# Kernel optimization log

Measured on AMD Instinct MI355X. Metric: run time of the kernel, lower is better.

Reference implementation:

```python
import jax, jax.numpy as jnp
import numpy as np
import math

D = 512
H = 8
DH = D // H
B, T = 4, 2048


def _poly(x, coeffs):
    # iterative-power polynomial eval, same products as the Vandermonde matmul
    acc = coeffs[0] * jnp.ones_like(x)
    p = jnp.ones_like(x)
    for i in range(1, coeffs.shape[0]):
        p = p * x
        acc = acc + coeffs[i] * p
    return acc


def _exp_fn(x, exp_c):
    return jnp.maximum(_poly(x, exp_c), 1e-8)


def _softmax(x, exp_c):
    x = x - jnp.max(x, axis=-1, keepdims=True)
    e = _exp_fn(x, exp_c)
    return e / jnp.sum(e, axis=-1, keepdims=True)


def _gelu(x, gelu_c):
    return _poly(jnp.clip(x, -4.0, 4.0), gelu_c)


def _layernorm(x, gamma, beta):
    mean = jnp.mean(x, axis=-1, keepdims=True)
    var = jnp.mean(x * x, axis=-1, keepdims=True) - mean * mean
    v = var + 1e-5
    y = jnp.full_like(v, 0.5)
    for _ in range(3):  # Newton iterations for rsqrt
        y = y * (3.0 - v * y * y) * 0.5
    return (x - mean) * y * gamma + beta


def setup_inputs() -> dict:
    key = jax.random.key(0)
    ks = jax.random.split(key, 8)
    x = jax.random.normal(ks[0], (B, T, D), dtype=jnp.float32)
    s = 0.02
    Wq = jax.random.normal(ks[1], (D, D), dtype=jnp.float32) * s
    Wk = jax.random.normal(ks[2], (D, D), dtype=jnp.float32) * s
    Wv = jax.random.normal(ks[3], (D, D), dtype=jnp.float32) * s
    Wo = jax.random.normal(ks[4], (D, D), dtype=jnp.float32) * s
    W1 = jax.random.normal(ks[5], (D, 4 * D), dtype=jnp.float32) * s
    W2 = jax.random.normal(ks[6], (4 * D, D), dtype=jnp.float32) * s
    g1 = jnp.ones((D,), jnp.float32); b1 = jnp.zeros((D,), jnp.float32)
    g2 = jnp.ones((D,), jnp.float32); b2 = jnp.zeros((D,), jnp.float32)
    # GELU degree-7 least-squares fit on [-4,4]
    x_fit = jnp.linspace(-4.0, 4.0, 1000)
    y_fit = 0.5 * x_fit * (1.0 + jax.scipy.special.erf(x_fit / math.sqrt(2.0)))
    V = x_fit[:, None] ** jnp.arange(8)[None, :]
    gelu_c = jnp.linalg.lstsq(V, y_fit)[0].astype(jnp.float32)
    # exp Taylor coeffs degree 6
    exp_c = jnp.array([1.0 / math.factorial(i) for i in range(7)], dtype=jnp.float32)
    return dict(x=x, Wq=Wq, Wk=Wk, Wv=Wv, Wo=Wo, W1=W1, W2=W2,
                g1=g1, b1=b1, g2=g2, b2=b2, gelu_c=gelu_c, exp_c=exp_c)


def reference(x, Wq, Wk, Wv, Wo, W1, W2, g1, b1, g2, b2, gelu_c, exp_c):
    Bn, Tn, Dn = x.shape
    q = (x @ Wq).reshape(Bn, Tn, H, DH).transpose(0, 2, 1, 3)  # [B,H,T,dh]
    k = (x @ Wk).reshape(Bn, Tn, H, DH).transpose(0, 2, 1, 3)
    v = (x @ Wv).reshape(Bn, Tn, H, DH).transpose(0, 2, 1, 3)
    scores = jnp.einsum('bhqd,bhkd->bhqk', q, k) / math.sqrt(DH)
    attn = _softmax(scores, exp_c)
    out = jnp.einsum('bhqk,bhkd->bhqd', attn, v).transpose(0, 2, 1, 3).reshape(Bn, Tn, Dn)
    out = out @ Wo
    h = _layernorm(x + out, g1, b1)
    ffn = _gelu(h @ W1, gelu_c) @ W2
    return _layernorm(h + ffn, g2, b2)
```

## Files before the change

kernel.cpp:

```cpp
#include <hip/hip_runtime.h>
#include <hip/hip_bf16.h>

typedef __bf16 bf16_t;
typedef __bf16 bf16x8 __attribute__((ext_vector_type(8)));
typedef float f32x4 __attribute__((ext_vector_type(4)));

#define MFMA16(a, b, c) __builtin_amdgcn_mfma_f32_16x16x32_bf16((a), (b), (c), 0, 0, 0)

__device__ __forceinline__ void gl_lds16(const bf16_t* g, bf16_t* l) {
  __builtin_amdgcn_global_load_lds(
      (const __attribute__((address_space(1))) void*)g,
      (__attribute__((address_space(3))) void*)l, 16, 0, 0);
}

__device__ __forceinline__ unsigned pack_bf16(float a, float b) {
  union { bf16_t h[2]; unsigned u; } c;
  c.h[0] = (bf16_t)a; c.h[1] = (bf16_t)b;
  return c.u;
}

__global__ __launch_bounds__(256) void k_prep(
    const float* __restrict__ x, bf16_t* __restrict__ x_bf,
    const float* __restrict__ Wq, const float* __restrict__ Wk,
    const float* __restrict__ Wv, const float* __restrict__ Wo,
    const float* __restrict__ W1, const float* __restrict__ W2,
    bf16_t* __restrict__ WqkvT, bf16_t* __restrict__ WoT,
    bf16_t* __restrict__ W1T, bf16_t* __restrict__ W2T) {
  __shared__ float tile[64][65];
  int bid = blockIdx.x, tid = threadIdx.x;
  if (bid < 4096) {
    int i = bid * 256 + tid;
    float4 f = ((const float4*)x)[i];
    union { bf16_t h[4]; uint2 u; } cv;
    cv.h[0] = (bf16_t)f.x; cv.h[1] = (bf16_t)f.y;
    cv.h[2] = (bf16_t)f.z; cv.h[3] = (bf16_t)f.w;
    ((uint2*)x_bf)[i] = cv.u;
    return;
  }
  int t = bid - 4096;
  const float* W; bf16_t* WT; int K, N, idx, gx;
  if (t < 64)       { W = Wq; WT = WqkvT;                      K = 512;  N = 512;  idx = t;       gx = 8;  }
  else if (t < 128) { W = Wk; WT = WqkvT + (size_t)512 * 512;  K = 512;  N = 512;  idx = t - 64;  gx = 8;  }
  else if (t < 192) { W = Wv; WT = WqkvT + (size_t)1024 * 512; K = 512;  N = 512;  idx = t - 128; gx = 8;  }
  else if (t < 256) { W = Wo; WT = WoT;                        K = 512;  N = 512;  idx = t - 192; gx = 8;  }
  else if (t < 512) { W = W1; WT = W1T;                        K = 512;  N = 2048; idx = t - 256; gx = 8;  }
  else              { W = W2; WT = W2T;                        K = 2048; N = 512;  idx = t - 512; gx = 32; }
  int bk = (idx % gx) * 64, bn = (idx / gx) * 64;
  int tx = tid & 63, ty = tid >> 6;
  for (int i = ty; i < 64; i += 4)
    tile[i][tx] = W[(size_t)(bk + i) * N + bn + tx];
  __syncthreads();
  for (int i = ty; i < 64; i += 4)
    WT[(size_t)(bn + i) * K + bk + tx] = (bf16_t)tile[tx][i];
}

template <int MODE, int BM>
__global__ __launch_bounds__(256) void k_gemm_bt(
    const bf16_t* __restrict__ A, const bf16_t* __restrict__ Bt,
    float* __restrict__ Cf, bf16_t* __restrict__ Cb,
    bf16_t* __restrict__ Cb2, bf16_t* __restrict__ Cb3,
    int M, int N, int K, const float* __restrict__ coef) {
  __shared__ __align__(16) bf16_t As[2][BM * 32];
  __shared__ __align__(16) bf16_t Bs[2][128 * 32];
  constexpr int NF = (BM == 128) ? 4 : 2;
  int tid = threadIdx.x;
  int lane = tid & 63, wave = tid >> 6;
  int bm = blockIdx.x * BM, bn = blockIdx.y * 128;
  int wr = (BM == 128) ? (wave >> 1) * 64 : 0;
  int wc = (BM == 128) ? (wave & 1) * 64 : wave * 32;
  int lr = lane & 15, lk = (lane >> 4) * 8;
  int srow = tid >> 2, scol = (tid & 3) * 8;

  f32x4 zero = {0.f, 0.f, 0.f, 0.f};
  f32x4 acc[4][NF];
#pragma unroll
  for (int m = 0; m < 4; ++m)
#pragma unroll
    for (int n = 0; n < NF; ++n) acc[m][n] = zero;

  const bf16_t* pA = A + (size_t)(bm + srow) * K + scol;
  const bf16_t* pB = Bt + (size_t)(bn + srow) * K + scol;

  auto STAGE = [&](int buf, int k0) {
    bf16_t* lA = &As[buf][tid * 8];
    bf16_t* lB = &Bs[buf][tid * 8];
    gl_lds16(pA + k0, lA);
    if (BM == 128) gl_lds16(pA + (size_t)64 * K + k0, lA + 2048);
    gl_lds16(pB + k0, lB);
    gl_lds16(pB + (size_t)64 * K + k0, lB + 2048);
  };

  STAGE(0, 0);
  __syncthreads();
  int buf = 0;
  for (int k0 = 0; k0 < K; k0 += 32) {
    if (k0 + 32 < K) STAGE(buf ^ 1, k0 + 32);
    bf16x8 a[4], b[NF];
#pragma unroll
    for (int m = 0; m < 4; ++m) a[m] = *(const bf16x8*)&As[buf][(wr + m * 16 + lr) * 32 + lk];
#pragma unroll
    for (int n = 0; n < NF; ++n) b[n] = *(const bf16x8*)&Bs[buf][(wc + n * 16 + lr) * 32 + lk];
    __builtin_amdgcn_s_setprio(1);
#pragma unroll
    for (int m = 0; m < 4; ++m)
#pragma unroll
      for (int n = 0; n < NF; ++n)
        acc[m][n] = MFMA16(a[m], b[n], acc[m][n]);
    __builtin_amdgcn_s_setprio(0);
    __syncthreads();
    buf ^= 1;
  }

  float c8[8];
  if (MODE == 4) {
#pragma unroll
    for (int i = 0; i < 8; ++i) c8[i] = coef[i];
  }
  int rbase = (lane >> 4) * 4;
#pragma unroll
  for (int m = 0; m < 4; ++m) {
#pragma unroll
    for (int n = 0; n < NF; ++n) {
#pragma unroll
      for (int r = 0; r < 4; ++r) {
        int gm = bm + wr + m * 16 + rbase + r;
        int gn = bn + wc + n * 16 + lr;
        float v = acc[m][n][r];
        if (MODE == 0) {
          Cf[(size_t)gm * N + gn] = v;
        } else if (MODE == 4) {
          float xx = fminf(fmaxf(v, -4.f), 4.f);
          float p = c8[0], pw = 1.f;
#pragma unroll
          for (int i = 1; i < 8; ++i) { pw *= xx; p += c8[i] * pw; }
          Cb[(size_t)gm * N + gn] = (bf16_t)p;
        } else {
          int mat = gn >> 9, col = gn & 511;
          int b_ = gm >> 11, t_ = gm & 2047, h_ = col >> 6, d_ = col & 63;
          if (mat == 0) {
            Cb[(((size_t)b_ * 8 + h_) * 2048 + t_) * 64 + d_] = (bf16_t)(v * 0.125f);
          } else if (mat == 1) {
            int dsw = d_ ^ ((t_ & 7) << 3);
            Cb2[(((size_t)b_ * 8 + h_) * 2048 + t_) * 64 + dsw] = (bf16_t)v;
          } else {
            int tw = t_ & 63;
            int j = (((tw >> 2) & 3) << 1) | ((tw >> 4) & 1);
            int phys = (((tw & 32) << 1) + (j << 3) + ((tw & 3) << 1)) ^ ((d_ & 7) << 4);
            size_t e = ((((size_t)b_ * 8 + h_) * 64 + d_) * 4096 +
                        (size_t)(t_ >> 6) * 128 + phys) >> 1;
            Cb3[e] = (bf16_t)v;
          }
        }
      }
    }
  }
}

__global__ __launch_bounds__(256, 4) void k_attn(
    const bf16_t* __restrict__ qb, const bf16_t* __restrict__ kb,
    const bf16_t* __restrict__ vtb, bf16_t* __restrict__ part,
    float* __restrict__ rsb, const float* __restrict__ exp_c) {
  __shared__ __align__(16) bf16_t Ks[2][64 * 64];
  __shared__ __align__(16) bf16_t Vs[2][64 * 64];
  int tid = threadIdx.x, lane = tid & 63, wave = tid >> 6;
  int b0 = blockIdx.x;
  int bid = (b0 & 7) * 128 + (b0 >> 3);
  int ks = bid & 1, qt = (bid >> 1) & 15, bh = bid >> 5;
  int kt0 = ks * 16;
  const size_t bho = (size_t)bh * (2048 * 64);
  const bf16_t* Q = qb + bho + (size_t)qt * 128 * 64;
  const bf16_t* Kp = kb + bho;
  const bf16_t* Vp = vtb + bho;
  int lr = lane & 15, lg = lane >> 4;

  bf16x8 qa[2][2];
#pragma unroll
  for (int j = 0; j < 2; ++j)
#pragma unroll
    for (int h = 0; h < 2; ++h)
      qa[j][h] = *(const bf16x8*)&Q[(wave * 32 + j * 16 + lr) * 64 + h * 32 + lg * 8];

  float ec[7];
#pragma unroll
  for (int i = 0; i < 7; ++i) ec[i] = exp_c[i];

  union { unsigned u[4]; bf16x8 v; } ones;
#pragma unroll
  for (int i = 0; i < 4; ++i) ones.u[i] = 0x3f803f80u;

  int offA[4], offB[4];
#pragma unroll
  for (int n = 0; n < 4; ++n) {
    int row = n * 16 + lr, sw = (row & 7) << 4;
    offA[n] = (row * 128 + lg * 16) ^ sw;
    offB[n] = (row * 128 + 64 + lg * 16) ^ sw;
  }

  auto STAGE_K = [&](int buf, int kt) {
    bf16_t* lk = &Ks[buf][tid * 8];
    const bf16_t* gk = Kp + (size_t)kt * 4096 + tid * 8;
    gl_lds16(gk, lk);
    gl_lds16(gk + 2048, lk + 2048);
  };
  auto STAGE_V = [&](int buf, int kt) {
    bf16_t* lv = &Vs[buf][tid * 8];
    const bf16_t* gv = Vp + (size_t)(tid >> 3) * 2048 + kt * 64 + (tid & 7) * 8;
    gl_lds16(gv, lv);
    gl_lds16(gv + (size_t)32 * 2048, lv + 2048);
  };

  f32x4 zero = {0.f, 0.f, 0.f, 0.f};
  f32x4 oacc[2][4], oacc_s[2];
#pragma unroll
  for (int j = 0; j < 2; ++j) {
#pragma unroll
    for (int n = 0; n < 4; ++n) oacc[j][n] = zero;
    oacc_s[j] = zero;
  }

  STAGE_K(0, kt0);
  STAGE_V(0, kt0);
  __syncthreads();

  for (int lt = 0; lt < 16; ++lt) {
    if (lt < 15) {
      STAGE_K((lt + 1) & 1, kt0 + lt + 1);
      STAGE_V((lt + 1) & 1, kt0 + lt + 1);
    }
    const char* kbase = (const char*)Ks[lt & 1];
    const char* vbase = (const char*)Vs[lt & 1];
    f32x4 s[2][4];
    __builtin_amdgcn_s_setprio(1);
#pragma unroll
    for (int n = 0; n < 4; ++n) {
      bf16x8 kb0 = *(const bf16x8*)(kbase + offA[n]);
      bf16x8 kb1 = *(const bf16x8*)(kbase + offB[n]);
#pragma unroll
      for (int j = 0; j < 2; ++j)
        s[j][n] = MFMA16(kb1, qa[j][1], MFMA16(kb0, qa[j][0], zero));
    }
    __builtin_amdgcn_s_setprio(0);
    union { unsigned u[4]; bf16x8 v; } pa[2][2];
#pragma unroll
    for (int j = 0; j < 2; ++j) {
      unsigned pk[4][2];
#pragma unroll
      for (int n = 0; n < 4; ++n) {
        float pf[4];
#pragma unroll
        for (int r = 0; r < 4; ++r) {
          float xv = s[j][n][r];
          float p = ec[6];
#pragma unroll
          for (int i = 5; i >= 0; --i) p = __builtin_fmaf(p, xv, ec[i]);
          pf[r] = p;
        }
        pk[n][0] = pack_bf16(pf[0], pf[1]);
        pk[n][1] = pack_bf16(pf[2], pf[3]);
      }
      pa[j][0].u[0] = pk[0][0]; pa[j][0].u[1] = pk[0][1];
      pa[j][0].u[2] = pk[1][0]; pa[j][0].u[3] = pk[1][1];
      pa[j][1].u[0] = pk[2][0]; pa[j][1].u[1] = pk[2][1];
      pa[j][1].u[2] = pk[3][0]; pa[j][1].u[3] = pk[3][1];
    }
    __builtin_amdgcn_s_setprio(1);
#pragma unroll
    for (int dd = 0; dd < 4; ++dd) {
      bf16x8 v0 = *(const bf16x8*)(vbase + offA[dd]);
      bf16x8 v1 = *(const bf16x8*)(vbase + offB[dd]);
#pragma unroll
      for (int j = 0; j < 2; ++j)
        oacc[j][dd] = MFMA16(pa[j][1].v, v1, MFMA16(pa[j][0].v, v0, oacc[j][dd]));
    }
#pragma unroll
    for (int j = 0; j < 2; ++j)
      oacc_s[j] = MFMA16(pa[j][1].v, ones.v, MFMA16(pa[j][0].v, ones.v, oacc_s[j]));
    __builtin_amdgcn_s_setprio(0);
    __syncthreads();
  }

  bf16_t* pp = part + (size_t)ks * (8192 * 512);
  int b_ = bh >> 3, h_ = bh & 7;
#pragma unroll
  for (int j = 0; j < 2; ++j) {
#pragma unroll
    for (int dd = 0; dd < 4; ++dd)
#pragma unroll
      for (int r = 0; r < 4; ++r) {
        int t_ = qt * 128 + wave * 32 + j * 16 + lg * 4 + r;
        int d_ = dd * 16 + lr;
        pp[(((size_t)b_ * 2048 + t_) * 8 + h_) * 64 + d_] = (bf16_t)oacc[j][dd][r];
      }
    if (lr == 0) {
#pragma unroll
      for (int r = 0; r < 4; ++r) {
        int t_ = qt * 128 + wave * 32 + j * 16 + lg * 4 + r;
        rsb[ks * 65536 + ((b_ * 2048 + t_) * 8 + h_)] = oacc_s[j][r];
      }
    }
  }
}

__global__ __launch_bounds__(256) void k_combine(
    const bf16_t* __restrict__ part, const float* __restrict__ rsb,
    bf16_t* __restrict__ ob) {
  int gid = blockIdx.x * 256 + threadIdx.x;
  int row = gid >> 3;
  float r = rsb[row] + rsb[65536 + row];
  bf16x8 a = ((const bf16x8*)part)[gid];
  bf16x8 b = ((const bf16x8*)(part + (size_t)8192 * 512))[gid];
  bf16x8 o;
#pragma unroll
  for (int i = 0; i < 8; ++i)
    o[i] = (bf16_t)(((float)a[i] + (float)b[i]) / r);
  ((bf16x8*)ob)[gid] = o;
}

template <int AB>
__global__ __launch_bounds__(256) void k_ln(
    const void* __restrict__ xav, const float* __restrict__ xb,
    const float* __restrict__ gamma, const float* __restrict__ beta,
    float* __restrict__ outf, bf16_t* __restrict__ outb) {
  int row = blockIdx.x * 4 + (threadIdx.x >> 6);
  int lane = threadIdx.x & 63;
  float xa[8];
  if (AB == 0) {
    const float* pa = (const float*)xav + (size_t)row * 512;
    float4 a0 = ((const float4*)pa)[lane];
    float4 a1 = ((const float4*)pa)[lane + 64];
    xa[0] = a0.x; xa[1] = a0.y; xa[2] = a0.z; xa[3] = a0.w;
    xa[4] = a1.x; xa[5] = a1.y; xa[6] = a1.z; xa[7] = a1.w;
  } else {
    const bf16_t* pa = (const bf16_t*)xav + (size_t)row * 512;
    union { uint2 u; bf16_t h[4]; } c0, c1;
    c0.u = ((const uint2*)pa)[lane];
    c1.u = ((const uint2*)pa)[lane + 64];
#pragma unroll
    for (int i = 0; i < 4; ++i) { xa[i] = (float)c0.h[i]; xa[4 + i] = (float)c1.h[i]; }
  }
  const float* pb = xb + (size_t)row * 512;
  float4 b0 = ((const float4*)pb)[lane];
  float4 b1 = ((const float4*)pb)[lane + 64];
  float x[8] = {xa[0] + b0.x, xa[1] + b0.y, xa[2] + b0.z, xa[3] + b0.w,
                xa[4] + b1.x, xa[5] + b1.y, xa[6] + b1.z, xa[7] + b1.w};
  float s = 0.f, sq = 0.f;
#pragma unroll
  for (int i = 0; i < 8; ++i) { s += x[i]; sq += x[i] * x[i]; }
#pragma unroll
  for (int off = 1; off < 64; off <<= 1) {
    s += __shfl_xor(s, off);
    sq += __shfl_xor(sq, off);
  }
  float mean = s * (1.f / 512.f);
  float var = sq * (1.f / 512.f) - mean * mean;
  float v = var + 1e-5f;
  float y = 0.5f;
#pragma unroll
  for (int it = 0; it < 3; ++it) y = y * (3.0f - v * y * y) * 0.5f;

  float4 g0 = ((const float4*)gamma)[lane];
  float4 g1 = ((const float4*)gamma)[lane + 64];
  float4 e0 = ((const float4*)beta)[lane];
  float4 e1 = ((const float4*)beta)[lane + 64];
  float o[8];
  o[0] = (x[0] - mean) * y * g0.x + e0.x;
  o[1] = (x[1] - mean) * y * g0.y + e0.y;
  o[2] = (x[2] - mean) * y * g0.z + e0.z;
  o[3] = (x[3] - mean) * y * g0.w + e0.w;
  o[4] = (x[4] - mean) * y * g1.x + e1.x;
  o[5] = (x[5] - mean) * y * g1.y + e1.y;
  o[6] = (x[6] - mean) * y * g1.z + e1.z;
  o[7] = (x[7] - mean) * y * g1.w + e1.w;
  if (outf) {
    float* po = outf + (size_t)row * 512;
    ((float4*)po)[lane]      = make_float4(o[0], o[1], o[2], o[3]);
    ((float4*)po)[lane + 64] = make_float4(o[4], o[5], o[6], o[7]);
  }
  if (outb) {
    bf16_t* pq = outb + (size_t)row * 512;
    union { bf16_t h[4]; uint2 u; } c0, c1;
    c0.h[0] = (bf16_t)o[0]; c0.h[1] = (bf16_t)o[1]; c0.h[2] = (bf16_t)o[2]; c0.h[3] = (bf16_t)o[3];
    c1.h[0] = (bf16_t)o[4]; c1.h[1] = (bf16_t)o[5]; c1.h[2] = (bf16_t)o[6]; c1.h[3] = (bf16_t)o[7];
    ((uint2*)pq)[lane]      = c0.u;
    ((uint2*)pq)[lane + 64] = c1.u;
  }
}

extern "C" void kernel_launch(void* const* d_in, const int* in_sizes, int n_in,
                              void* d_out, int out_size, void* d_ws, size_t ws_size,
                              hipStream_t stream) {
  const float* x      = (const float*)d_in[0];
  const float* Wq     = (const float*)d_in[1];
  const float* Wk     = (const float*)d_in[2];
  const float* Wv     = (const float*)d_in[3];
  const float* Wo     = (const float*)d_in[4];
  const float* W1     = (const float*)d_in[5];
  const float* W2     = (const float*)d_in[6];
  const float* g1     = (const float*)d_in[7];
  const float* b1     = (const float*)d_in[8];
  const float* g2     = (const float*)d_in[9];
  const float* b2     = (const float*)d_in[10];
  const float* gelu_c = (const float*)d_in[11];
  const float* exp_c  = (const float*)d_in[12];

  const int M = 8192;
  const size_t actBF = (size_t)M * 512 * 2;
  char* p = (char*)d_ws;
  auto carve = [&](size_t bytes) {
    void* r = (void*)p;
    p += (bytes + 255) & ~(size_t)255;
    return r;
  };
  bf16_t* x_bf   = (bf16_t*)carve(actBF);
  bf16_t* q_bf   = (bf16_t*)carve(actBF);
  bf16_t* k_bf   = (bf16_t*)carve(actBF);
  bf16_t* vT_bf  = (bf16_t*)carve(actBF);
  bf16_t* o_bf   = (bf16_t*)carve(actBF);
  bf16_t* h_bf   = (bf16_t*)carve(actBF);
  bf16_t* WqkvT  = (bf16_t*)carve((size_t)1536 * 512 * 2);
  bf16_t* WoT    = (bf16_t*)carve(512 * 512 * 2);
  bf16_t* W1T    = (bf16_t*)carve(512 * 2048 * 2);
  bf16_t* W2T    = (bf16_t*)carve(512 * 2048 * 2);
  bf16_t* g_bf   = (bf16_t*)carve((size_t)M * 2048 * 2);
  float*  proj   = (float*)carve((size_t)M * 512 * 4);
  float*  f2     = proj;
  bf16_t* part   = (bf16_t*)g_bf;
  float*  rsb    = (float*)proj;

  k_prep<<<4864, 256, 0, stream>>>(x, x_bf, Wq, Wk, Wv, Wo, W1, W2,
                                   WqkvT, WoT, W1T, W2T);

  k_gemm_bt<5, 128><<<dim3(64, 12), 256, 0, stream>>>(
      x_bf, WqkvT, nullptr, q_bf, k_bf, vT_bf, M, 1536, 512, nullptr);

  k_attn<<<1024, 256, 0, stream>>>(q_bf, k_bf, vT_bf, part, rsb, exp_c);

  k_combine<<<2048, 256, 0, stream>>>(part, rsb, o_bf);

  k_gemm_bt<0, 64><<<dim3(128, 4), 256, 0, stream>>>(
      o_bf, WoT, proj, nullptr, nullptr, nullptr, M, 512, 512, nullptr);

  k_ln<0><<<2048, 256, 0, stream>>>(x, proj, g1, b1, nullptr, h_bf);

  k_gemm_bt<4, 128><<<dim3(64, 16), 256, 0, stream>>>(
      h_bf, W1T, nullptr, g_bf, nullptr, nullptr, M, 2048, 512, gelu_c);

  k_gemm_bt<0, 64><<<dim3(128, 4), 256, 0, stream>>>(
      g_bf, W2T, f2, nullptr, nullptr, nullptr, M, 512, 2048, nullptr);

  k_ln<1><<<2048, 256, 0, stream>>>(h_bf, f2, g2, b2, (float*)d_out, nullptr);
}
```

Baseline: 187.8 us.

## Add dedicated 256x256-tile FFN1 GEMM kernel with multi-stage LDS pipeline

Replaces the generic GEMM used for the first FFN matmul (with GELU epilogue) with a specialized kernel. It uses 512-thread blocks, 256x256 output tiles and 128KB of dynamic LDS. A four-buffer global_load_lds pipeline, explicit vmcnt waits and barriers interleave the next loads with the MFMA phases. The aim is more data reuse per tile and better overlap of memory traffic with compute. The grid drops to 256 blocks and the kernel needs a large shared-memory allocation, so occupancy is low and the hand-written waitcnt sequencing is fragile.

New measurement: 182.6 us, median of 2. 1.03x faster.

```diff
diff --git a/kernel.cpp b/kernel.cpp
--- a/kernel.cpp
+++ b/kernel.cpp
@@ -111,11 +111,6 @@
     buf ^= 1;
   }
 
-  float c8[8];
-  if (MODE == 4) {
-#pragma unroll
-    for (int i = 0; i < 8; ++i) c8[i] = coef[i];
-  }
   int rbase = (lane >> 4) * 4;
 #pragma unroll
   for (int m = 0; m < 4; ++m) {
@@ -128,12 +123,6 @@
         float v = acc[m][n][r];
         if (MODE == 0) {
           Cf[(size_t)gm * N + gn] = v;
-        } else if (MODE == 4) {
-          float xx = fminf(fmaxf(v, -4.f), 4.f);
-          float p = c8[0], pw = 1.f;
-#pragma unroll
-          for (int i = 1; i < 8; ++i) { pw *= xx; p += c8[i] * pw; }
-          Cb[(size_t)gm * N + gn] = (bf16_t)p;
         } else {
           int mat = gn >> 9, col = gn & 511;
           int b_ = gm >> 11, t_ = gm & 2047, h_ = col >> 6, d_ = col & 63;
@@ -153,6 +142,110 @@
         }
       }
     }
+  }
+}
+
+__global__ __launch_bounds__(512, 2) void k_ffn1(
+    const bf16_t* __restrict__ A, const bf16_t* __restrict__ Bt,
+    bf16_t* __restrict__ C, const float* __restrict__ coef) {
+  extern __shared__ __align__(16) bf16_t ldsraw[];
+  int tid = threadIdx.x;
+  int lane = tid & 63, wave = tid >> 6;
+  int wm = wave >> 2, wn = wave & 3;
+  int lr = lane & 15, lg = lane >> 4;
+  int bm = blockIdx.x * 256, bn = blockIdx.y * 256;
+
+  f32x4 zero = {0.f, 0.f, 0.f, 0.f};
+  f32x4 acc[8][4];
+#pragma unroll
+  for (int a = 0; a < 8; ++a)
+#pragma unroll
+    for (int n = 0; n < 4; ++n) acc[a][n] = zero;
+
+  int srow = tid >> 2, scol = (tid & 3) * 8;
+  const bf16_t* gA = A + (size_t)(bm + srow) * 512 + scol;
+  const bf16_t* gB = Bt + (size_t)(bn + srow) * 512 + scol;
+
+  auto LBASE = [&](int slot, int op, int kh) -> bf16_t* {
+    return ldsraw + (size_t)((((slot << 1) | op) << 1) | kh) * 8192;
+  };
+  auto STG = [&](int slot, int op, int kh, int kt) {
+    if (kt >= 8) return;
+    bf16_t* dst = LBASE(slot, op, kh) + tid * 8;
+    const bf16_t* src = (op ? gB : gA) + kt * 64 + kh * 32;
+    gl_lds16(src, dst);
+    gl_lds16(src + (size_t)128 * 512, dst + 4096);
+  };
+
+  auto PH = [&](int slot, int kh, int qm, int sS, int sOp, int sKh, int sT, bool vm) {
+    bf16x8 af[4], bb[4];
+    const bf16_t* Abase = LBASE(slot, 0, kh);
+    const bf16_t* Bbase = LBASE(slot, 1, kh);
+#pragma unroll
+    for (int mf = 0; mf < 4; ++mf) {
+      int r = wm * 128 + qm * 64 + mf * 16 + lr;
+      af[mf] = *(const bf16x8*)&Abase[r * 32 + lg * 8];
+    }
+#pragma unroll
+    for (int nf = 0; nf < 4; ++nf) {
+      int r = wn * 64 + nf * 16 + lr;
+      bb[nf] = *(const bf16x8*)&Bbase[r * 32 + lg * 8];
+    }
+    STG(sS, sOp, sKh, sT);
+    if (vm) __asm__ volatile("s_waitcnt vmcnt(6)" ::: "memory");
+    __asm__ volatile("" ::: "memory");
+    __builtin_amdgcn_s_barrier();
+    __asm__ volatile("" ::: "memory");
+    __builtin_amdgcn_s_setprio(1);
+#pragma unroll
+    for (int mf = 0; mf < 4; ++mf)
+#pragma unroll
+      for (int nf = 0; nf < 4; ++nf)
+        acc[qm * 4 + mf][nf] = MFMA16(af[mf], bb[nf], acc[qm * 4 + mf][nf]);
+    __builtin_amdgcn_s_setprio(0);
+    __asm__ volatile("" ::: "memory");
+    __builtin_amdgcn_s_barrier();
+    __asm__ volatile("" ::: "memory");
+  };
+
+  STG(0, 0, 0, 0); STG(0, 1, 0, 0); STG(0, 0, 1, 0); STG(0, 1, 1, 0);
+  STG(1, 0, 0, 1); STG(1, 1, 0, 1);
+  __asm__ volatile("s_waitcnt vmcnt(8)" ::: "memory");
+  __builtin_amdgcn_s_barrier();
+  __asm__ volatile("" ::: "memory");
+
+#pragma unroll
+  for (int i = 0; i < 4; ++i) {
+    int t1 = 2 * i + 1;
+    PH(0, 0, 0, 1, 0, 1, t1, false);
+    PH(0, 0, 1, 1, 1, 1, t1, true);
+    PH(0, 1, 0, 0, 0, 0, t1 + 1, false);
+    PH(0, 1, 1, 0, 1, 0, t1 + 1, true);
+    PH(1, 0, 0, 0, 0, 1, t1 + 1, false);
+    PH(1, 0, 1, 0, 1, 1, t1 + 1, true);
+    PH(1, 1, 0, 1, 0, 0, t1 + 2, false);
+    PH(1, 1, 1, 1, 1, 0, t1 + 2, true);
+  }
+
+  float c8[8];
+#pragma unroll
+  for (int q = 0; q < 8; ++q) c8[q] = coef[q];
+#pragma unroll
+  for (int am = 0; am < 8; ++am) {
+    int qm = am >> 2, mf = am & 3;
+#pragma unroll
+    for (int nf = 0; nf < 4; ++nf)
+#pragma unroll
+      for (int rr = 0; rr < 4; ++rr) {
+        int row = bm + wm * 128 + qm * 64 + mf * 16 + lg * 4 + rr;
+        int col = bn + wn * 64 + nf * 16 + lr;
+        float v = acc[am][nf][rr];
+        float xx = fminf(fmaxf(v, -4.f), 4.f);
+        float pw = 1.f, pp = c8[0];
+#pragma unroll
+        for (int q2 = 1; q2 < 8; ++q2) { pw *= xx; pp += c8[q2] * pw; }
+        C[(size_t)row * 2048 + col] = (bf16_t)pp;
+      }
   }
 }
 
@@ -442,8 +535,7 @@
 
   k_ln<0><<<2048, 256, 0, stream>>>(x, proj, g1, b1, nullptr, h_bf);
 
-  k_gemm_bt<4, 128><<<dim3(64, 16), 256, 0, stream>>>(
-      h_bf, W1T, nullptr, g_bf, nullptr, nullptr, M, 2048, 512, gelu_c);
+  k_ffn1<<<dim3(32, 8), 512, 131072, stream>>>(h_bf, W1T, g_bf, gelu_c);
 
   k_gemm_bt<0, 64><<<dim3(128, 4), 256, 0, stream>>>(
       g_bf, W2T, f2, nullptr, nullptr, nullptr, M, 512, 2048, nullptr);
```
